# Kernel optimization log

Hardware: AMD Instinct MI355X
Metric: run time of the kernel (lower is better)

The kernel has to match this reference:

```python
import jax, jax.numpy as jnp
import numpy as np

# Keras GRUCell (reset_after=True, default in TF2) step
# Keras LSTMCell step (gate order i, f, c, o)
# Keras RNN masking semantics: at masked steps, states are frozen and the
# step output is the previous output (equivalent to freezing every layer's h).

def _gru_step(a, h, W, U, bi, br):
    gx = a @ W + bi          # [B, 3H] input projection
    gh = h @ U + br          # [B, 3H] recurrent projection (reset_after)
    xz, xr, xh = jnp.split(gx, 3, axis=-1)
    rz, rr, rh = jnp.split(gh, 3, axis=-1)
    z = jax.nn.sigmoid(xz + rz)
    r = jax.nn.sigmoid(xr + rr)
    hh = jnp.tanh(xh + r * rh)
    return z * h + (1.0 - z) * hh


def _lstm_step(a, h, c, W, U, b):
    g = a @ W + h @ U + b    # [B, 4H]
    gi, gf, gc, go = jnp.split(g, 4, axis=-1)
    i = jax.nn.sigmoid(gi)
    f = jax.nn.sigmoid(gf)
    cn = f * c + i * jnp.tanh(gc)
    hn = jax.nn.sigmoid(go) * jnp.tanh(cn)
    return hn, cn


def run_gru_stack(x, mask, layers):
    # x: [B,T,D], mask: [B,T] bool; layers: list of (W,U,bi,br)
    B = x.shape[0]
    H = layers[0][1].shape[0]
    xT = jnp.swapaxes(x, 0, 1)      # [T,B,D]
    mT = jnp.swapaxes(mask, 0, 1)   # [T,B]

    def step(hs, inp):
        xt, mt = inp
        a = xt
        new = []
        for (W, U, bi, br), h in zip(layers, hs):
            hn = _gru_step(a, h, W, U, bi, br)
            hn = jnp.where(mt[:, None], hn, h)  # freeze state under mask
            new.append(hn)
            a = hn
        return tuple(new), a

    h0 = tuple(jnp.zeros((B, H), x.dtype) for _ in layers)
    _, ys = jax.lax.scan(step, h0, (xT, mT))
    return jnp.swapaxes(ys, 0, 1)   # [B,T,H]


def run_lstm_stack(x, mask, layers):
    # layers: list of (W,U,b)
    B = x.shape[0]
    H = layers[0][1].shape[0]
    xT = jnp.swapaxes(x, 0, 1)
    mT = jnp.swapaxes(mask, 0, 1)

    def step(state, inp):
        xt, mt = inp
        a = xt
        new = []
        for (W, U, b), (h, c) in zip(layers, state):
            hn, cn = _lstm_step(a, h, c, W, U, b)
            hn = jnp.where(mt[:, None], hn, h)
            cn = jnp.where(mt[:, None], cn, c)
            new.append((hn, cn))
            a = hn
        return tuple(new), a

    s0 = tuple((jnp.zeros((B, H), x.dtype), jnp.zeros((B, H), x.dtype)) for _ in layers)
    _, ys = jax.lax.scan(step, s0, (xT, mT))
    return jnp.swapaxes(ys, 0, 1)


def _forward(x, lengths, g_W0, g_U0, g_bi0, g_br0, g_W1, g_U1, g_bi1, g_br1,
             l_W0, l_U0, l_b0, l_W1, l_U1, l_b1, out_W, out_b):
    T = x.shape[1]
    mask = jnp.arange(T)[None, :] < lengths[:, None]          # [B,T]
    o1 = run_gru_stack(x, mask, [(g_W0, g_U0, g_bi0, g_br0),
                                 (g_W1, g_U1, g_bi1, g_br1)])  # [B,T,H]
    o2 = run_lstm_stack(x, mask, [(l_W0, l_U0, l_b0),
                                  (l_W1, l_U1, l_b1)])          # [B,T,H]
    c = jnp.concatenate([o1, o2], axis=-1)                      # [B,T,2H]
    return c @ out_W + out_b                                    # [B,T,1]


def setup_inputs() -> dict:
    key = jax.random.key(0)
    ks = jax.random.split(key, 16)
    B, T, D, H = 64, 512, 96, 256
    glorot = lambda k, shp: (jax.random.normal(k, shp, dtype=jnp.float32)
                             / np.sqrt(shp[0]).astype(np.float32))
    inp = {
        "x": jax.random.normal(ks[0], (B, T, D), dtype=jnp.float32),
        "lengths": jax.random.randint(ks[1], (B,), 1, T + 1),
        # GRU stack (reset_after: separate input/recurrent biases)
        "g_W0": glorot(ks[2], (D, 3 * H)),
        "g_U0": glorot(ks[3], (H, 3 * H)),
        "g_bi0": jnp.zeros((3 * H,), jnp.float32),
        "g_br0": jnp.zeros((3 * H,), jnp.float32),
        "g_W1": glorot(ks[4], (H, 3 * H)),
        "g_U1": glorot(ks[5], (H, 3 * H)),
        "g_bi1": jnp.zeros((3 * H,), jnp.float32),
        "g_br1": jnp.zeros((3 * H,), jnp.float32),
        # LSTM stack
        "l_W0": glorot(ks[6], (D, 4 * H)),
        "l_U0": glorot(ks[7], (H, 4 * H)),
        "l_b0": jnp.zeros((4 * H,), jnp.float32),
        "l_W1": glorot(ks[8], (H, 4 * H)),
        "l_U1": glorot(ks[9], (H, 4 * H)),
        "l_b1": jnp.zeros((4 * H,), jnp.float32),
        # Dense head on concat [.., 2H] -> 1
        "out_W": glorot(ks[10], (2 * H, 1)),
        "out_b": jnp.zeros((1,), jnp.float32),
    }
    return inp


def reference(x, lengths, g_W0, g_U0, g_bi0, g_br0, g_W1, g_U1, g_bi1, g_br1,
              l_W0, l_U0, l_b0, l_W1, l_U1, l_b1, out_W, out_b):
    return _forward(x, lengths, g_W0, g_U0, g_bi0, g_br0, g_W1, g_U1, g_bi1,
                    g_br1, l_W0, l_U0, l_b0, l_W1, l_U1, l_b1, out_W, out_b)
```

## Files before the change

kernel.cpp:

```cpp
#include <hip/hip_runtime.h>
#include <hip/hip_fp16.h>

constexpr int Tt = 512, Dd = 96, Hh = 256;
constexpr int NS0 = 16;
constexpr int NSP = 8;
typedef unsigned long long u64;

constexpr size_t OFF_P0  = (size_t)4 << 20;
constexpr size_t OFF_P1  = (size_t)12 << 20;
constexpr size_t OFF_FLG = (size_t)20 << 20;
constexpr size_t OFF_W16 = ((size_t)20 << 20) + ((size_t)64 << 10);
constexpr size_t oGW0 = 0;
constexpr size_t oGU0 = oGW0 + (size_t)48 * 768;
constexpr size_t oGW1 = oGU0 + (size_t)128 * 768;
constexpr size_t oGU1 = oGW1 + (size_t)128 * 768;
constexpr size_t oLW0 = oGU1 + (size_t)128 * 768;
constexpr size_t oLU0 = oLW0 + (size_t)48 * 1024;
constexpr size_t oLW1 = oLU0 + (size_t)128 * 1024;
constexpr size_t oLU1 = oLW1 + (size_t)128 * 1024;

__device__ __forceinline__ float sigf(float v) { return 1.0f / (1.0f + __expf(-v)); }
__device__ __forceinline__ u64 agld(const u64* p) {
    return __hip_atomic_load(p, __ATOMIC_RELAXED, __HIP_MEMORY_SCOPE_AGENT);
}
__device__ __forceinline__ int agldi(const int* p) {
    return __hip_atomic_load(p, __ATOMIC_ACQUIRE, __HIP_MEMORY_SCOPE_AGENT);
}
__device__ __forceinline__ void agst(u64* p, u64 v) {
    __hip_atomic_store(p, v, __ATOMIC_RELAXED, __HIP_MEMORY_SCOPE_AGENT);
}

__device__ __forceinline__ float dot2f(unsigned w, unsigned a, float acc) {
#if __has_builtin(__builtin_amdgcn_fdot2)
    typedef _Float16 h2v __attribute__((ext_vector_type(2)));
    h2v wh, ah;
    __builtin_memcpy(&wh, &w, 4);
    __builtin_memcpy(&ah, &a, 4);
    return __builtin_amdgcn_fdot2(wh, ah, acc, false);
#else
    const float2 wf = __half22float2(*(const __half2*)&w);
    const float2 af = __half22float2(*(const __half2*)&a);
    acc = fmaf(wf.x, af.x, acc);
    return fmaf(wf.y, af.y, acc);
#endif
}

__device__ __forceinline__ int hidx(int k, int r) {
    return (k >> 1) * 8 + r * 2 + (k & 1);
}

template<int G>
__device__ __forceinline__ void load4h(uint4* wv, const uint4* __restrict__ M4,
                                       int ldm, int kpb) {
    const int base = (kpb >> 2) * ldm;
    #pragma unroll
    for (int g = 0; g < G; ++g)
        wv[g] = M4[base + g * 256];
}
template<int G>
__device__ __forceinline__ void fma4h(const uint4* wv, const uint4* __restrict__ A4,
                                      int kpb, float4* acc) {
    const uint4 a0 = A4[kpb + 0];
    const uint4 a1 = A4[kpb + 1];
    const uint4 a2 = A4[kpb + 2];
    const uint4 a3 = A4[kpb + 3];
    #pragma unroll
    for (int g = 0; g < G; ++g) {
        const uint4 w = wv[g];
        acc[g].x = dot2f(w.x, a0.x, acc[g].x);
        acc[g].y = dot2f(w.x, a0.y, acc[g].y);
        acc[g].z = dot2f(w.x, a0.z, acc[g].z);
        acc[g].w = dot2f(w.x, a0.w, acc[g].w);
        acc[g].x = dot2f(w.y, a1.x, acc[g].x);
        acc[g].y = dot2f(w.y, a1.y, acc[g].y);
        acc[g].z = dot2f(w.y, a1.z, acc[g].z);
        acc[g].w = dot2f(w.y, a1.w, acc[g].w);
        acc[g].x = dot2f(w.z, a2.x, acc[g].x);
        acc[g].y = dot2f(w.z, a2.y, acc[g].y);
        acc[g].z = dot2f(w.z, a2.z, acc[g].z);
        acc[g].w = dot2f(w.z, a2.w, acc[g].w);
        acc[g].x = dot2f(w.w, a3.x, acc[g].x);
        acc[g].y = dot2f(w.w, a3.y, acc[g].y);
        acc[g].z = dot2f(w.w, a3.z, acc[g].z);
        acc[g].w = dot2f(w.w, a3.w, acc[g].w);
    }
}
template<int G>
__device__ __forceinline__ void gemmP(const uint4* __restrict__ M4, int ldm,
                                      const uint4* __restrict__ A4,
                                      int kp0, int kp1, float4* acc) {
    const int n4 = (kp1 - kp0) >> 2;
    uint4 wv0[G], wv1[G];
    if (n4 <= 0) return;
    load4h<G>(wv0, M4, ldm, kp0);
    int c2 = 0;
    for (; c2 + 2 <= n4; c2 += 2) {
        load4h<G>(wv1, M4, ldm, kp0 + (c2 + 1) * 4);
        fma4h<G>(wv0, A4, kp0 + c2 * 4, acc);
        if (c2 + 2 < n4) load4h<G>(wv0, M4, ldm, kp0 + (c2 + 2) * 4);
        fma4h<G>(wv1, A4, kp0 + (c2 + 1) * 4, acc);
    }
    if (c2 < n4) fma4h<G>(wv0, A4, kp0 + c2 * 4, acc);
}

__global__ void cvt_pair(const float* __restrict__ src, unsigned* __restrict__ dst,
                         int n, int ld) {
    const int i = blockIdx.x * 256 + threadIdx.x;
    if (i >= n) return;
    const int kp = i / ld, col = i - kp * ld;
    const __half2 h = __floats2half2_rn(src[(2 * kp) * ld + col],
                                        src[(2 * kp + 1) * ld + col]);
    dst[((size_t)((kp >> 2) * ld + col) << 2) + (kp & 3)] = *(const unsigned*)&h;
}

__global__ void __launch_bounds__(512, 1)
rnn_persist(const float* __restrict__ x, const int* __restrict__ lengths,
            const float* __restrict__ gbi0, const float* __restrict__ gbr0,
            const float* __restrict__ gbi1, const float* __restrict__ gbr1,
            const float* __restrict__ lb0, const float* __restrict__ lb1,
            const float* __restrict__ outW, const float* __restrict__ outb,
            float* __restrict__ out, char* __restrict__ wsb)
{
    const int tid = threadIdx.x;
    const int c   = tid & 255;
    const int grp = tid >> 8;
    const int bx  = blockIdx.x;
    const int role  = bx & 3;
    const int chain = (bx >> 2) & 1;
    const int rg    = bx >> 3;
    const int rowbase = rg * 4;

    const int GA  = chain ? 4 : 3;
    const int GAH = GA * Hh;

    u64* h0ring = (u64*)wsb + (size_t)(chain * 16 + rg) * (NS0 * 1024);
    u64* p0ring = (u64*)(wsb + OFF_P0) + (size_t)(chain * 16 + rg) * (NSP * 4096);
    u64* p1ring = (u64*)(wsb + OFF_P1) + (size_t)(chain * 16 + rg) * (NSP * 4096);
    int* flags = (int*)(wsb + OFF_FLG);
    int* flg_r0 = flags + ((chain * 16 + rg) * 4 + 1) * 32;
    int* flg_p1 = flags + ((chain * 16 + rg) * 4 + 2) * 32;
    int* flg_r1 = flags + ((chain * 16 + rg) * 4 + 3) * 32;

    const unsigned* W16 = (const unsigned*)(wsb + OFF_W16);
    size_t woff;
    if (chain == 0) woff = (role == 0) ? oGW0 : (role == 1) ? oGU0 : (role == 2) ? oGW1 : oGU1;
    else            woff = (role == 0) ? oLW0 : (role == 1) ? oLU0 : (role == 2) ? oLW1 : oLU1;
    const uint4* M4 = (const uint4*)(W16 + woff) + c;

    const int KR  = (role == 0) ? Dd : Hh;
    const int KP2 = KR >> 2;
    const int kp0 = grp * KP2, kp1 = kp0 + KP2;

    __shared__ __align__(16) unsigned sAh[128 * 4];
    __shared__ float sG[2 * 4096];
    __shared__ float sP[4096];
    __shared__ float sRed[16];
    __half* sAhh = (__half*)sAh;
    const uint4* A4 = (const uint4*)sAh;

    const int NP  = 4 * GAH;
    const int npt = NP >> 9;
    float biasv[8];
    int sgidx[8];
    if (role == 0 || role == 2) {
        const float* bsrc = (chain == 0) ? (role == 0 ? gbi0 : gbi1)
                                         : (role == 0 ? lb0 : lb1);
        #pragma unroll
        for (int i = 0; i < 8; ++i) {
            if (i < npt) {
                const int e = tid + i * 512;
                const int r = e / GAH, rem = e - r * GAH;
                biasv[i] = bsrc[rem];
                sgidx[i] = r * 1024 + rem;
            } else { biasv[i] = 0; sgidx[i] = 0; }
        }
    }
    const int rA = tid >> 8;
    const int lenA = lengths[rowbase + rA];
    const int lenB = lengths[rowbase + rA + 2];
    float brz = 0, brr = 0, brh = 0, ow = 0;
    if (chain == 0 && (role == 1 || role == 3)) {
        const float* br = (role == 1) ? gbr0 : gbr1;
        brz = br[c]; brr = br[Hh + c]; brh = br[2 * Hh + c];
    }
    if (role == 3) ow = outW[chain * Hh + c];
    const float outb0 = outb[0];
    float creg0 = 0.0f, creg1 = 0.0f;
    float hprev0 = 0.0f, hprev1 = 0.0f;

    for (int i = tid; i < 512; i += 512) sAh[i] = 0;
    __syncthreads();

    for (int t = 0; t < Tt; ++t) {
        if (role == 0) {
            if (t >= NSP) {
                if (tid == 0)
                    while (agldi(flg_r0) < t - NSP + 1) __builtin_amdgcn_s_sleep(1);
                __syncthreads();
            }
            if (tid < 4 * Dd) {
                const int r = tid / Dd, k = tid - r * Dd;
                const float v = x[((size_t)(rowbase + r) * Tt + t) * Dd + k];
                sAhh[hidx(k, r)] = __float2half(v);
            }
            __syncthreads();
        } else if (role == 2) {
            const u64* base = h0ring + (size_t)(t & (NS0 - 1)) * 1024;
            const unsigned want = (unsigned)(t + 1);
            const int r0i = rA, r1i = rA + 2;
            const u64* p0 = base + r0i * 256 + c;
            const u64* p1 = base + r1i * 256 + c;
            u64 v0 = 0, v1 = 0; bool d0 = false, d1 = false;
            do {
                if (!d0) { v0 = agld(p0); d0 = ((unsigned)v0 == want); }
                if (!d1) { v1 = agld(p1); d1 = ((unsigned)v1 == want); }
            } while (!(d0 && d1));
            sAhh[hidx(c, r0i)] = __float2half(__uint_as_float((unsigned)(v0 >> 32)));
            sAhh[hidx(c, r1i)] = __float2half(__uint_as_float((unsigned)(v1 >> 32)));
            __syncthreads();
            if (tid == 0)
                __hip_atomic_exchange(flg_p1, t + 1, __ATOMIC_RELEASE,
                                      __HIP_MEMORY_SCOPE_AGENT);
        } else {
            const u64* slot = ((role == 1) ? p0ring : p1ring)
                              + (size_t)(t & (NSP - 1)) * 4096;
            const unsigned want = (unsigned)(t + 1);
            unsigned dm = 0;
            const unsigned full = (1u << npt) - 1u;
            while (dm != full) {
                for (int i = 0; i < npt; ++i) {
                    if (!(dm & (1u << i))) {
                        const u64 v = agld(slot + tid + i * 512);
                        if ((unsigned)v == want) {
                            sP[tid + i * 512] = __uint_as_float((unsigned)(v >> 32));
                            dm |= 1u << i;
                        }
                    }
                }
            }
            __syncthreads();
            if (tid == 0)
                __hip_atomic_exchange((role == 1) ? flg_r0 : flg_r1, t + 1,
                                      __ATOMIC_RELEASE, __HIP_MEMORY_SCOPE_AGENT);
        }

        {
            if (chain == 0) {
                float4 acc[3] = {{0,0,0,0},{0,0,0,0},{0,0,0,0}};
                gemmP<3>(M4, GAH, A4, kp0, kp1, acc);
                #pragma unroll
                for (int g = 0; g < 3; ++g) {
                    sG[grp * 4096 + 0 + g * 256 + c]    = acc[g].x;
                    sG[grp * 4096 + 1024 + g * 256 + c] = acc[g].y;
                    sG[grp * 4096 + 2048 + g * 256 + c] = acc[g].z;
                    sG[grp * 4096 + 3072 + g * 256 + c] = acc[g].w;
                }
            } else {
                float4 acc[4] = {{0,0,0,0},{0,0,0,0},{0,0,0,0},{0,0,0,0}};
                gemmP<4>(M4, GAH, A4, kp0, kp1, acc);
                #pragma unroll
                for (int g = 0; g < 4; ++g) {
                    sG[grp * 4096 + 0 + g * 256 + c]    = acc[g].x;
                    sG[grp * 4096 + 1024 + g * 256 + c] = acc[g].y;
                    sG[grp * 4096 + 2048 + g * 256 + c] = acc[g].z;
                    sG[grp * 4096 + 3072 + g * 256 + c] = acc[g].w;
                }
            }
        }
        __syncthreads();

        if (role == 0 || role == 2) {
            if (role == 2 && t >= NSP) {
                if (tid == 0)
                    while (agldi(flg_r1) < t - NSP + 1) __builtin_amdgcn_s_sleep(1);
                __syncthreads();
            }
            u64* ring = (role == 0) ? p0ring : p1ring;
            u64* slot = ring + (size_t)(t & (NSP - 1)) * 4096;
            for (int i = 0; i < npt; ++i) {
                const float v = sG[sgidx[i]] + sG[4096 + sgidx[i]] + biasv[i];
                agst(slot + tid + i * 512,
                     ((u64)__float_as_uint(v) << 32) | (unsigned)(t + 1));
            }
        } else {
            if (role == 1 && t >= NS0) {
                if (tid == 0)
                    while (agldi(flg_p1) < t - NS0 + 1) __builtin_amdgcn_s_sleep(1);
                __syncthreads();
            }
            float vh0 = 0.0f, vh1 = 0.0f;
            #pragma unroll
            for (int e = 0; e < 2; ++e) {
                const int r = rA + e * 2;
                const float hold = e ? hprev1 : hprev0;
                const int len = e ? lenB : lenA;
                float hn;
                if (chain == 0) {
                    const float Pz = sP[r * GAH + c];
                    const float Pr = sP[r * GAH + Hh + c];
                    const float Ph = sP[r * GAH + 2 * Hh + c];
                    const float Qz = sG[r * 1024 + c]       + sG[4096 + r * 1024 + c];
                    const float Qr = sG[r * 1024 + 256 + c] + sG[4096 + r * 1024 + 256 + c];
                    const float Qh = sG[r * 1024 + 512 + c] + sG[4096 + r * 1024 + 512 + c];
                    const float z  = sigf(Pz + Qz + brz);
                    const float rr = sigf(Pr + Qr + brr);
                    const float hh = tanhf(Ph + rr * (Qh + brh));
                    hn = z * hold + (1.0f - z) * hh;
                    if (t >= len) hn = hold;
                } else {
                    const float gi = sP[r * GAH + c]          + sG[r * 1024 + c]       + sG[4096 + r * 1024 + c];
                    const float gf = sP[r * GAH + Hh + c]     + sG[r * 1024 + 256 + c] + sG[4096 + r * 1024 + 256 + c];
                    const float gc = sP[r * GAH + 2 * Hh + c] + sG[r * 1024 + 512 + c] + sG[4096 + r * 1024 + 512 + c];
                    const float go = sP[r * GAH + 3 * Hh + c] + sG[r * 1024 + 768 + c] + sG[4096 + r * 1024 + 768 + c];
                    const float cold = e ? creg1 : creg0;
                    float cn = sigf(gf) * cold + sigf(gi) * tanhf(gc);
                    hn = sigf(go) * tanhf(cn);
                    if (t >= len) { hn = hold; cn = cold; }
                    if (e) creg1 = cn; else creg0 = cn;
                }
                if (e) hprev1 = hn; else hprev0 = hn;
                sAhh[hidx(c, r)] = __float2half(hn);
                if (role == 1) {
                    agst(h0ring + (size_t)(t & (NS0 - 1)) * 1024 + r * 256 + c,
                         ((u64)__float_as_uint(hn) << 32) | (unsigned)(t + 1));
                } else {
                    if (e) vh1 = hn * ow; else vh0 = hn * ow;
                }
            }
            if (role == 3) {
                const int w = tid >> 6;
                for (int o = 32; o > 0; o >>= 1) {
                    vh0 += __shfl_down(vh0, o);
                    vh1 += __shfl_down(vh1, o);
                }
                if ((tid & 63) == 0) { sRed[w] = vh0; sRed[8 + w] = vh1; }
                __syncthreads();
                if (tid < 4) {
                    const float s = sRed[tid * 4] + sRed[tid * 4 + 1]
                                  + sRed[tid * 4 + 2] + sRed[tid * 4 + 3];
                    atomicAdd(&out[(size_t)(rowbase + tid) * Tt + t],
                              s + (chain ? outb0 : 0.0f));
                }
            }
        }
        __syncthreads();
    }
}

extern "C" void kernel_launch(void* const* d_in, const int* in_sizes, int n_in,
                              void* d_out, int out_size, void* d_ws, size_t ws_size,
                              hipStream_t stream) {
    const float* x       = (const float*)d_in[0];
    const int*   lengths = (const int*)d_in[1];
    const float* gW0  = (const float*)d_in[2];
    const float* gU0  = (const float*)d_in[3];
    const float* gbi0 = (const float*)d_in[4];
    const float* gbr0 = (const float*)d_in[5];
    const float* gW1  = (const float*)d_in[6];
    const float* gU1  = (const float*)d_in[7];
    const float* gbi1 = (const float*)d_in[8];
    const float* gbr1 = (const float*)d_in[9];
    const float* lW0  = (const float*)d_in[10];
    const float* lU0  = (const float*)d_in[11];
    const float* lb0  = (const float*)d_in[12];
    const float* lW1  = (const float*)d_in[13];
    const float* lU1  = (const float*)d_in[14];
    const float* lb1  = (const float*)d_in[15];
    const float* outW = (const float*)d_in[16];
    const float* outb = (const float*)d_in[17];
    float* out = (float*)d_out;
    char* wsb  = (char*)d_ws;

    hipMemsetAsync(d_ws, 0, OFF_FLG + (16 << 10), stream);
    hipMemsetAsync(d_out, 0, (size_t)out_size * sizeof(float), stream);

    unsigned* W16 = (unsigned*)(wsb + OFF_W16);
    struct { const float* s; size_t o; int K; int ld; } cv[8] = {
        {gW0, oGW0, 96, 768}, {gU0, oGU0, 256, 768},
        {gW1, oGW1, 256, 768}, {gU1, oGU1, 256, 768},
        {lW0, oLW0, 96, 1024}, {lU0, oLU0, 256, 1024},
        {lW1, oLW1, 256, 1024}, {lU1, oLU1, 256, 1024},
    };
    for (int i = 0; i < 8; ++i) {
        const int n = (cv[i].K / 2) * cv[i].ld;
        cvt_pair<<<(n + 255) / 256, 256, 0, stream>>>(cv[i].s, W16 + cv[i].o, n, cv[i].ld);
    }

    rnn_persist<<<dim3(128), dim3(512), 0, stream>>>(
        x, lengths, gbi0, gbr0, gbi1, gbr1, lb0, lb1, outW, outb, out, wsb);
}
```

Baseline: 5.836 ms.

## Double block size to 1024 threads, splitting K four ways with shared-memory reduction

Each persistent block now runs 1024 threads. The recurrent GEMV's K dimension is split across four thread groups instead of two, with the partial sums combined in shared memory through an extra barrier. In the elementwise gate stage each thread now handles a single batch row instead of two, and the polling and ring indexing are updated to match. The goal is to shorten the serial per-step latency by spreading work over more waves, at the cost of an extra __syncthreads, read-modify-write on shared memory, and tighter register limits under the new launch bounds.

```diff
diff --git a/kernel.cpp b/kernel.cpp
--- a/kernel.cpp
+++ b/kernel.cpp
@@ -113,7 +113,7 @@
     dst[((size_t)((kp >> 2) * ld + col) << 2) + (kp & 3)] = *(const unsigned*)&h;
 }
 
-__global__ void __launch_bounds__(512, 1)
+__global__ void __launch_bounds__(1024, 4)
 rnn_persist(const float* __restrict__ x, const int* __restrict__ lengths,
             const float* __restrict__ gbi0, const float* __restrict__ gbr0,
             const float* __restrict__ gbi1, const float* __restrict__ gbr1,
@@ -148,7 +148,7 @@
     const uint4* M4 = (const uint4*)(W16 + woff) + c;
 
     const int KR  = (role == 0) ? Dd : Hh;
-    const int KP2 = KR >> 2;
+    const int KP2 = KR >> 3;
     const int kp0 = grp * KP2, kp1 = kp0 + KP2;
 
     __shared__ __align__(16) unsigned sAh[128 * 4];
@@ -159,25 +159,24 @@
     const uint4* A4 = (const uint4*)sAh;
 
     const int NP  = 4 * GAH;
-    const int npt = NP >> 9;
-    float biasv[8];
-    int sgidx[8];
+    const int npt = NP >> 10;
+    float biasv[4];
+    int sgidx[4];
     if (role == 0 || role == 2) {
         const float* bsrc = (chain == 0) ? (role == 0 ? gbi0 : gbi1)
                                          : (role == 0 ? lb0 : lb1);
         #pragma unroll
-        for (int i = 0; i < 8; ++i) {
+        for (int i = 0; i < 4; ++i) {
             if (i < npt) {
-                const int e = tid + i * 512;
+                const int e = tid + i * 1024;
                 const int r = e / GAH, rem = e - r * GAH;
                 biasv[i] = bsrc[rem];
                 sgidx[i] = r * 1024 + rem;
             } else { biasv[i] = 0; sgidx[i] = 0; }
         }
     }
-    const int rA = tid >> 8;
+    const int rA = grp;
     const int lenA = lengths[rowbase + rA];
-    const int lenB = lengths[rowbase + rA + 2];
     float brz = 0, brr = 0, brh = 0, ow = 0;
     if (chain == 0 && (role == 1 || role == 3)) {
         const float* br = (role == 1) ? gbr0 : gbr1;
@@ -185,10 +184,10 @@
     }
     if (role == 3) ow = outW[chain * Hh + c];
     const float outb0 = outb[0];
-    float creg0 = 0.0f, creg1 = 0.0f;
-    float hprev0 = 0.0f, hprev1 = 0.0f;
-
-    for (int i = tid; i < 512; i += 512) sAh[i] = 0;
+    float creg = 0.0f;
+    float hprev = 0.0f;
+
+    for (int i = tid; i < 512; i += 1024) sAh[i] = 0;
     __syncthreads();
 
     for (int t = 0; t < Tt; ++t) {
@@ -205,18 +204,11 @@
             }
             __syncthreads();
         } else if (role == 2) {
-            const u64* base = h0ring + (size_t)(t & (NS0 - 1)) * 1024;
+            const u64* p0 = h0ring + (size_t)(t & (NS0 - 1)) * 1024 + rA * 256 + c;
             const unsigned want = (unsigned)(t + 1);
-            const int r0i = rA, r1i = rA + 2;
-            const u64* p0 = base + r0i * 256 + c;
-            const u64* p1 = base + r1i * 256 + c;
-            u64 v0 = 0, v1 = 0; bool d0 = false, d1 = false;
-            do {
-                if (!d0) { v0 = agld(p0); d0 = ((unsigned)v0 == want); }
-                if (!d1) { v1 = agld(p1); d1 = ((unsigned)v1 == want); }
-            } while (!(d0 && d1));
-            sAhh[hidx(c, r0i)] = __float2half(__uint_as_float((unsigned)(v0 >> 32)));
-            sAhh[hidx(c, r1i)] = __float2half(__uint_as_float((unsigned)(v1 >> 32)));
+            u64 v0;
+            do { v0 = agld(p0); } while ((unsigned)v0 != want);
+            sAhh[hidx(c, rA)] = __float2half(__uint_as_float((unsigned)(v0 >> 32)));
             __syncthreads();
             if (tid == 0)
                 __hip_atomic_exchange(flg_p1, t + 1, __ATOMIC_RELEASE,
@@ -230,9 +222,9 @@
             while (dm != full) {
                 for (int i = 0; i < npt; ++i) {
                     if (!(dm & (1u << i))) {
-                        const u64 v = agld(slot + tid + i * 512);
+                        const u64 v = agld(slot + tid + i * 1024);
                         if ((unsigned)v == want) {
-                            sP[tid + i * 512] = __uint_as_float((unsigned)(v >> 32));
+                            sP[tid + i * 1024] = __uint_as_float((unsigned)(v >> 32));
                             dm |= 1u << i;
                         }
                     }
@@ -244,10 +236,10 @@
                                       __ATOMIC_RELEASE, __HIP_MEMORY_SCOPE_AGENT);
         }
 
-        {
-            if (chain == 0) {
-                float4 acc[3] = {{0,0,0,0},{0,0,0,0},{0,0,0,0}};
-                gemmP<3>(M4, GAH, A4, kp0, kp1, acc);
+        if (chain == 0) {
+            float4 acc[3] = {{0,0,0,0},{0,0,0,0},{0,0,0,0}};
+            gemmP<3>(M4, GAH, A4, kp0, kp1, acc);
+            if (grp < 2) {
                 #pragma unroll
                 for (int g = 0; g < 3; ++g) {
                     sG[grp * 4096 + 0 + g * 256 + c]    = acc[g].x;
@@ -255,9 +247,22 @@
                     sG[grp * 4096 + 2048 + g * 256 + c] = acc[g].z;
                     sG[grp * 4096 + 3072 + g * 256 + c] = acc[g].w;
                 }
-            } else {
-                float4 acc[4] = {{0,0,0,0},{0,0,0,0},{0,0,0,0},{0,0,0,0}};
-                gemmP<4>(M4, GAH, A4, kp0, kp1, acc);
+            }
+            __syncthreads();
+            if (grp >= 2) {
+                const int b = (grp - 2) * 4096;
+                #pragma unroll
+                for (int g = 0; g < 3; ++g) {
+                    sG[b + 0 + g * 256 + c]    += acc[g].x;
+                    sG[b + 1024 + g * 256 + c] += acc[g].y;
+                    sG[b + 2048 + g * 256 + c] += acc[g].z;
+                    sG[b + 3072 + g * 256 + c] += acc[g].w;
+                }
+            }
+        } else {
+            float4 acc[4] = {{0,0,0,0},{0,0,0,0},{0,0,0,0},{0,0,0,0}};
+            gemmP<4>(M4, GAH, A4, kp0, kp1, acc);
+            if (grp < 2) {
                 #pragma unroll
                 for (int g = 0; g < 4; ++g) {
                     sG[grp * 4096 + 0 + g * 256 + c]    = acc[g].x;
@@ -266,6 +271,17 @@
                     sG[grp * 4096 + 3072 + g * 256 + c] = acc[g].w;
                 }
             }
+            __syncthreads();
+            if (grp >= 2) {
+                const int b = (grp - 2) * 4096;
+                #pragma unroll
+                for (int g = 0; g < 4; ++g) {
+                    sG[b + 0 + g * 256 + c]    += acc[g].x;
+                    sG[b + 1024 + g * 256 + c] += acc[g].y;
+                    sG[b + 2048 + g * 256 + c] += acc[g].z;
+                    sG[b + 3072 + g * 256 + c] += acc[g].w;
+                }
+            }
         }
         __syncthreads();
 
@@ -279,7 +295,7 @@
             u64* slot = ring + (size_t)(t & (NSP - 1)) * 4096;
             for (int i = 0; i < npt; ++i) {
                 const float v = sG[sgidx[i]] + sG[4096 + sgidx[i]] + biasv[i];
-                agst(slot + tid + i * 512,
+                agst(slot + tid + i * 1024,
                      ((u64)__float_as_uint(v) << 32) | (unsigned)(t + 1));
             }
         } else {
@@ -288,52 +304,41 @@
                     while (agldi(flg_p1) < t - NS0 + 1) __builtin_amdgcn_s_sleep(1);
                 __syncthreads();
             }
-            float vh0 = 0.0f, vh1 = 0.0f;
-            #pragma unroll
-            for (int e = 0; e < 2; ++e) {
-                const int r = rA + e * 2;
-                const float hold = e ? hprev1 : hprev0;
-                const int len = e ? lenB : lenA;
-                float hn;
-                if (chain == 0) {
-                    const float Pz = sP[r * GAH + c];
-                    const float Pr = sP[r * GAH + Hh + c];
-                    const float Ph = sP[r * GAH + 2 * Hh + c];
-                    const float Qz = sG[r * 1024 + c]       + sG[4096 + r * 1024 + c];
-                    const float Qr = sG[r * 1024 + 256 + c] + sG[4096 + r * 1024 + 256 + c];
-                    const float Qh = sG[r * 1024 + 512 + c] + sG[4096 + r * 1024 + 512 + c];
-                    const float z  = sigf(Pz + Qz + brz);
-                    const float rr = sigf(Pr + Qr + brr);
-                    const float hh = tanhf(Ph + rr * (Qh + brh));
-                    hn = z * hold + (1.0f - z) * hh;
-                    if (t >= len) hn = hold;
-                } else {
-                    const float gi = sP[r * GAH + c]          + sG[r * 1024 + c]       + sG[4096 + r * 1024 + c];
-                    const float gf = sP[r * GAH + Hh + c]     + sG[r * 1024 + 256 + c] + sG[4096 + r * 1024 + 256 + c];
-                    const float gc = sP[r * GAH + 2 * Hh + c] + sG[r * 1024 + 512 + c] + sG[4096 + r * 1024 + 512 + c];
-                    const float go = sP[r * GAH + 3 * Hh + c] + sG[r * 1024 + 768 + c] + sG[4096 + r * 1024 + 768 + c];
-                    const float cold = e ? creg1 : creg0;
-                    float cn = sigf(gf) * cold + sigf(gi) * tanhf(gc);
-                    hn = sigf(go) * tanhf(cn);
-                    if (t >= len) { hn = hold; cn = cold; }
-                    if (e) creg1 = cn; else creg0 = cn;
-                }
-                if (e) hprev1 = hn; else hprev0 = hn;
-                sAhh[hidx(c, r)] = __float2half(hn);
-                if (role == 1) {
-                    agst(h0ring + (size_t)(t & (NS0 - 1)) * 1024 + r * 256 + c,
-                         ((u64)__float_as_uint(hn) << 32) | (unsigned)(t + 1));
-                } else {
-                    if (e) vh1 = hn * ow; else vh0 = hn * ow;
-                }
-            }
-            if (role == 3) {
-                const int w = tid >> 6;
-                for (int o = 32; o > 0; o >>= 1) {
-                    vh0 += __shfl_down(vh0, o);
-                    vh1 += __shfl_down(vh1, o);
-                }
-                if ((tid & 63) == 0) { sRed[w] = vh0; sRed[8 + w] = vh1; }
+            const int r = rA;
+            const float hold = hprev;
+            float hn;
+            if (chain == 0) {
+                const float Pz = sP[r * GAH + c];
+                const float Pr = sP[r * GAH + Hh + c];
+                const float Ph = sP[r * GAH + 2 * Hh + c];
+                const float Qz = sG[r * 1024 + c]       + sG[4096 + r * 1024 + c];
+                const float Qr = sG[r * 1024 + 256 + c] + sG[4096 + r * 1024 + 256 + c];
+                const float Qh = sG[r * 1024 + 512 + c] + sG[4096 + r * 1024 + 512 + c];
+                const float z  = sigf(Pz + Qz + brz);
+                const float rr = sigf(Pr + Qr + brr);
+                const float hh = tanhf(Ph + rr * (Qh + brh));
+                hn = z * hold + (1.0f - z) * hh;
+                if (t >= lenA) hn = hold;
+            } else {
+                const float gi = sP[r * GAH + c]          + sG[r * 1024 + c]       + sG[4096 + r * 1024 + c];
+                const float gf = sP[r * GAH + Hh + c]     + sG[r * 1024 + 256 + c] + sG[4096 + r * 1024 + 256 + c];
+                const float gc = sP[r * GAH + 2 * Hh + c] + sG[r * 1024 + 512 + c] + sG[4096 + r * 1024 + 512 + c];
+                const float go = sP[r * GAH + 3 * Hh + c] + sG[r * 1024 + 768 + c] + sG[4096 + r * 1024 + 768 + c];
+                float cn = sigf(gf) * creg + sigf(gi) * tanhf(gc);
+                hn = sigf(go) * tanhf(cn);
+                if (t >= lenA) { hn = hold; cn = creg; }
+                creg = cn;
+            }
+            hprev = hn;
+            sAhh[hidx(c, r)] = __float2half(hn);
+            if (role == 1) {
+                agst(h0ring + (size_t)(t & (NS0 - 1)) * 1024 + r * 256 + c,
+                     ((u64)__float_as_uint(hn) << 32) | (unsigned)(t + 1));
+            } else {
+                float vh = hn * ow;
+                for (int o = 32; o > 0; o >>= 1)
+                    vh += __shfl_down(vh, o);
+                if ((tid & 63) == 0) sRed[tid >> 6] = vh;
                 __syncthreads();
                 if (tid < 4) {
                     const float s = sRed[tid * 4] + sRed[tid * 4 + 1]
@@ -386,6 +391,6 @@
         cvt_pair<<<(n + 255) / 256, 256, 0, stream>>>(cv[i].s, W16 + cv[i].o, n, cv[i].ld);
     }
 
-    rnn_persist<<<dim3(128), dim3(512), 0, stream>>>(
+    rnn_persist<<<dim3(128), dim3(1024), 0, stream>>>(
         x, lengths, gbi0, gbr0, gbi1, gbr1, lb0, lb1, outW, outb, out, wsb);
 }
```

Result: faster. 5.410 ms (-7.3%).
